# Kernel optimization log

Hardware: AMD Instinct MI355X
Metric: run time of the kernel (lower is better)

Reference implementation:

```python
import jax, jax.numpy as jnp
import numpy as np

CHUNK = 4096
DECAY = 0.99
EPS = 1e-5


def setup_inputs() -> dict:
    key = jax.random.key(0)
    k1, k2, k3, k4 = jax.random.split(key, 4)
    z = jax.random.normal(k1, (32, 64, 32, 32), dtype=jnp.float32)
    codebook = jax.random.normal(k2, (8192, 64), dtype=jnp.float32)
    cluster_size = jax.random.uniform(k3, (8192,), dtype=jnp.float32)
    embed_avg = jax.random.normal(k4, (8192, 64), dtype=jnp.float32)
    return {"z": z, "codebook": codebook, "cluster_size": cluster_size, "embed_avg": embed_avg}


def _nearest_indices(vectors, codebook):
    """Chunked fp32 squared-L2 nearest-neighbor search (matches _nearest_indices)."""
    cb = codebook.astype(jnp.float32)
    c2 = jnp.sum(cb * cb, axis=1)  # [K]

    def chunk_fn(chunk):
        v = chunk.astype(jnp.float32)  # [CHUNK, D]
        d = jnp.sum(v * v, axis=1, keepdims=True) + c2[None, :] - 2.0 * (v @ cb.T)
        return jnp.argmin(d, axis=1)

    n, d = vectors.shape  # n divisible by CHUNK by construction
    chunks = vectors.reshape(n // CHUNK, CHUNK, d)
    return jax.lax.map(chunk_fn, chunks).reshape(-1)


def reference(z, codebook, cluster_size, embed_avg):
    B, C, H, W = z.shape
    K = codebook.shape[0]
    # [B,C,H,W] -> [N,C]
    vectors = jnp.transpose(z, (0, 2, 3, 1)).reshape(-1, C)
    N = vectors.shape[0]

    indices = _nearest_indices(vectors, codebook)  # [N] int
    quantized = jnp.transpose(codebook[indices].reshape(B, H, W, C), (0, 3, 1, 2))

    # commitment loss (codebook learned via EMA, so only encoder side differentiable)
    vq_loss = jnp.mean((jax.lax.stop_gradient(quantized) - z) ** 2)
    # straight-through estimator
    quantized_st = z + jax.lax.stop_gradient(quantized - z)

    # code usage statistics
    counts = jax.ops.segment_sum(jnp.ones((N,), jnp.float32), indices, num_segments=K)
    avg_probs = counts / N
    perplexity = jnp.exp(-jnp.sum(avg_probs * jnp.log(avg_probs + 1e-10)))
    active_codes = jnp.sum(counts > 0).astype(jnp.int32)

    # EMA update (scatter-add accumulation + Laplace-smoothed normalization)
    sums = jax.ops.segment_sum(vectors.astype(jnp.float32), indices, num_segments=K)
    new_cluster_size = DECAY * cluster_size + (1.0 - DECAY) * counts
    new_embed_avg = DECAY * embed_avg + (1.0 - DECAY) * sums
    n_total = jnp.sum(new_cluster_size)
    smoothed = (new_cluster_size + EPS) / (n_total + K * EPS) * n_total
    new_codebook = new_embed_avg / smoothed[:, None]

    return (quantized_st, indices, vq_loss, perplexity, active_codes,
            new_codebook, new_cluster_size, new_embed_avg)
```

## Files before the change

### kernel.cpp

```cpp
#include <hip/hip_runtime.h>
#include <math.h>

typedef unsigned short u16;
typedef unsigned int u32;
typedef unsigned long long u64;
typedef __attribute__((ext_vector_type(8))) short short8;
typedef __attribute__((ext_vector_type(4))) float f32x4;

#define NVEC   32768
#define DIMV   64
#define KC     8192
#define NKCH   8
#define CHK    1024
#define HW     1024
#define BPLANE 65536
#define NSTEP  (CHK / 32)

#define OFF_Q    0
#define OFF_IDX  2097152
#define OFF_LOSS 2129920
#define OFF_PPL  2129921
#define OFF_ACT  2129922
#define OFF_NCB  2129923
#define OFF_NCS  2654211
#define OFF_NEA  2662403

#define WS_COUNTS 0
#define WS_SCAL   8192
#define WS_C2     8200
#define WS_MINP   16400
#define WS_OFFS   81936
#define WS_PERM   90128
#define WS_CBF    122896

__device__ __forceinline__ u16 f2bf(float x) {
    u32 u = __float_as_uint(x);
    u += 0x7fffu + ((u >> 16) & 1u);
    return (u16)(u >> 16);
}
__device__ __forceinline__ float bf2f(u16 h) {
    return __uint_as_float(((u32)h) << 16);
}
__device__ __forceinline__ u32 fmono(float f) {
    u32 b = __float_as_uint(f);
    return (b & 0x80000000u) ? ~b : (b | 0x80000000u);
}

__global__ __launch_bounds__(256) void cbsplit_kernel(const float* __restrict__ cb,
                                                      u16* __restrict__ cbf,
                                                      float* __restrict__ c2,
                                                      float* __restrict__ counts,
                                                      float* __restrict__ scal,
                                                      u64* __restrict__ minp) {
    const int t = threadIdx.x;
    const int gid = blockIdx.x * 256 + t;
    if (gid < 8192) counts[gid] = 0.f;
    if (gid < 8) scal[gid] = 0.f;
    if (gid < NVEC) minp[gid] = ~0ull;

    const int k = blockIdx.x * 4 + (t >> 6);
    const int d = t & 63;
    const int idx = k * DIMV + d;
    float x = cb[idx];
    u16 hb = f2bf(x);  float fh = bf2f(hb);
    float r1 = x - fh; u16 mb = f2bf(r1); float fm = bf2f(mb);
    float r2 = r1 - fm; u16 lb = f2bf(r2);
    const int ti = k >> 4, row = k & 15;
    const int half = d >> 5;
    const int cg = (d >> 3) & 3;
    const int le = row + cg * 16;
    u16* base = cbf + (size_t)ti * 3072 + le * 8 + (d & 7);
    base[(0 + half) * 512] = hb;
    base[(2 + half) * 512] = mb;
    base[(4 + half) * 512] = lb;
    float s = x * x;
    for (int off = 32; off > 0; off >>= 1) s += __shfl_down(s, off, 64);
    if (d == 0) c2[k] = s;
}

#define NN_COMPUTE(Bh0, Bh1, Bm0, Bm1, Bl0, Bl1, CM, NTI)                          \
    _Pragma("unroll")                                                               \
    for (int i = 0; i < 2; ++i) {                                                   \
        f32x4 acc = {CM, CM, CM, CM};                                               \
        acc = __builtin_amdgcn_mfma_f32_16x16x32_bf16(A[i][0][0], Bh0, acc, 0, 0, 0);\
        acc = __builtin_amdgcn_mfma_f32_16x16x32_bf16(A[i][0][1], Bh1, acc, 0, 0, 0);\
        acc = __builtin_amdgcn_mfma_f32_16x16x32_bf16(A[i][1][0], Bh0, acc, 0, 0, 0);\
        acc = __builtin_amdgcn_mfma_f32_16x16x32_bf16(A[i][1][1], Bh1, acc, 0, 0, 0);\
        acc = __builtin_amdgcn_mfma_f32_16x16x32_bf16(A[i][0][0], Bm0, acc, 0, 0, 0);\
        acc = __builtin_amdgcn_mfma_f32_16x16x32_bf16(A[i][0][1], Bm1, acc, 0, 0, 0);\
        acc = __builtin_amdgcn_mfma_f32_16x16x32_bf16(A[i][1][0], Bm0, acc, 0, 0, 0);\
        acc = __builtin_amdgcn_mfma_f32_16x16x32_bf16(A[i][1][1], Bm1, acc, 0, 0, 0);\
        acc = __builtin_amdgcn_mfma_f32_16x16x32_bf16(A[i][2][0], Bh0, acc, 0, 0, 0);\
        acc = __builtin_amdgcn_mfma_f32_16x16x32_bf16(A[i][2][1], Bh1, acc, 0, 0, 0);\
        acc = __builtin_amdgcn_mfma_f32_16x16x32_bf16(A[i][0][0], Bl0, acc, 0, 0, 0);\
        acc = __builtin_amdgcn_mfma_f32_16x16x32_bf16(A[i][0][1], Bl1, acc, 0, 0, 0);\
        _Pragma("unroll")                                                           \
        for (int r = 0; r < 4; ++r) {                                               \
            float a = acc[r];                                                       \
            if (a > bestv[i][r]) { bestv[i][r] = a; bestn[i][r] = (NTI); }          \
        }                                                                           \
    }

#define STAGE(B, ST)                                                                \
    _Pragma("unroll")                                                               \
    for (int j = 0; j < 3; ++j) {                                                   \
        const u16* gs = pcbf + (size_t)(ST) * 6144 + j * 2048 + tl * 8;             \
        u16* ld = &ldsb[B][j * 2048 + wv * 512];                                    \
        __builtin_amdgcn_global_load_lds(                                           \
            (const __attribute__((address_space(1))) void*)gs,                      \
            (__attribute__((address_space(3))) void*)ld, 16, 0, 0);                 \
    }

__global__ __launch_bounds__(256, 4) void nn_kernel(const float* __restrict__ z,
                                                    const u16* __restrict__ cbf,
                                                    const float* __restrict__ c2,
                                                    u64* __restrict__ minp) {
    __shared__ __align__(16) u16 ldsb[2][6144];
    const int tl = threadIdx.x;
    const int l  = tl & 63;
    const int wv = tl >> 6;
    const int vg = blockIdx.x;
    const int kc = blockIdx.y;
    const int m0 = vg * 128 + wv * 32;
    const int lr = l & 15;
    const int lg = l >> 4;

    short8 A[2][3][2];
#pragma unroll
    for (int i = 0; i < 2; ++i) {
        const int vec = m0 + i * 16 + lr;
        const float* zp = z + (size_t)(vec >> 10) * BPLANE + (vec & 1023);
#pragma unroll
        for (int s = 0; s < 2; ++s) {
            short8 ah, am, al;
#pragma unroll
            for (int e = 0; e < 8; ++e) {
                const int k = s * 32 + lg * 8 + e;
                float x = zp[k * HW];
                u16 hb = f2bf(x);   float fh = bf2f(hb);
                float r1 = x - fh;  u16 mb = f2bf(r1); float fm = bf2f(mb);
                float r2 = r1 - fm; u16 lb = f2bf(r2);
                ah[e] = (short)hb; am[e] = (short)mb; al[e] = (short)lb;
            }
            A[i][0][s] = ah; A[i][1][s] = am; A[i][2][s] = al;
        }
    }

    float bestv[2][4];
    int   bestn[2][4];
#pragma unroll
    for (int i = 0; i < 2; ++i)
#pragma unroll
        for (int r = 0; r < 4; ++r) { bestv[i][r] = -3.4e38f; bestn[i][r] = 0; }

    const int code_base = kc * CHK;
    const float* pc2 = c2 + code_base + lr;
    const u16* pcbf = cbf + (size_t)kc * (CHK / 16) * 3072;

    STAGE(0, 0)
    __syncthreads();

    for (int st = 0; st < NSTEP; ++st) {
        const int b = st & 1;
        const float cmA = -0.5f * pc2[(st * 2) * 16];
        const float cmB = -0.5f * pc2[(st * 2 + 1) * 16];
        if (st + 1 < NSTEP) { STAGE(b ^ 1, st + 1) }

        const u16* baseA = &ldsb[b][l * 8];
        {
            short8 h0 = *(const short8*)(baseA);
            short8 h1 = *(const short8*)(baseA + 512);
            short8 m0f = *(const short8*)(baseA + 1024);
            short8 m1f = *(const short8*)(baseA + 1536);
            short8 l0f = *(const short8*)(baseA + 2048);
            short8 l1f = *(const short8*)(baseA + 2560);
            NN_COMPUTE(h0, h1, m0f, m1f, l0f, l1f, cmA, st * 2)
        }
        {
            const u16* baseB = baseA + 3072;
            short8 h0 = *(const short8*)(baseB);
            short8 h1 = *(const short8*)(baseB + 512);
            short8 m0f = *(const short8*)(baseB + 1024);
            short8 m1f = *(const short8*)(baseB + 1536);
            short8 l0f = *(const short8*)(baseB + 2048);
            short8 l1f = *(const short8*)(baseB + 2560);
            NN_COMPUTE(h0, h1, m0f, m1f, l0f, l1f, cmB, st * 2 + 1)
        }
        __syncthreads();
    }

#pragma unroll
    for (int i = 0; i < 2; ++i)
#pragma unroll
        for (int r = 0; r < 4; ++r) {
            float v = bestv[i][r];
            int idx = bestn[i][r] * 16 + lr;
#pragma unroll
            for (int mk = 1; mk < 16; mk <<= 1) {
                float ov = __shfl_xor(v, mk, 64);
                int   oi = __shfl_xor(idx, mk, 64);
                if (ov > v || (ov == v && oi < idx)) { v = ov; idx = oi; }
            }
            if (lr == 0) {
                const int vec = m0 + i * 16 + lg * 4 + r;
                const u64 pack = ((u64)fmono(-v) << 32) | (u32)(code_base + idx);
                atomicMin(&minp[vec], pack);
            }
        }
}

__global__ __launch_bounds__(256) void gather_kernel(const float* __restrict__ z,
                                                     const float* __restrict__ cb,
                                                     const u64* __restrict__ minp,
                                                     float* __restrict__ out,
                                                     float* __restrict__ counts,
                                                     float* __restrict__ scal) {
    const int n = blockIdx.x * 256 + threadIdx.x;
    const int bi = (int)(u32)(minp[n] & 0xFFFFFFFFu);
    out[OFF_IDX + n] = (float)bi;
    atomicAdd(&counts[bi], 1.0f);

    const int b = n >> 10, h = n & 1023;
    const float* zp = z + (size_t)b * BPLANE + h;
    const float* cp = cb + (size_t)bi * DIMV;
    float* qp = out + OFF_Q + (size_t)b * BPLANE + h;
    float acc = 0.f;
#pragma unroll
    for (int c = 0; c < DIMV; ++c) {
        float zv = zp[c * HW];
        float q = cp[c];
        float df = q - zv;
        acc = fmaf(df, df, acc);
        qp[c * HW] = zv + df;
    }
    for (int off = 32; off > 0; off >>= 1) acc += __shfl_down(acc, off, 64);
    __shared__ float red[4];
    if ((threadIdx.x & 63) == 0) red[threadIdx.x >> 6] = acc;
    __syncthreads();
    if (threadIdx.x == 0) atomicAdd(&scal[0], (red[0] + red[1]) + (red[2] + red[3]));
}

__global__ __launch_bounds__(256) void prefix_kernel(const float* __restrict__ counts,
                                                     const float* __restrict__ cs,
                                                     float* __restrict__ out,
                                                     int* __restrict__ offs,
                                                     float* __restrict__ scal) {
    __shared__ int part[256];
    __shared__ float r0[4], r1[4], r2[4];
    const int t = threadIdx.x;
    const int base = t * 32;
    int loc[32];
    int s = 0;
    float sncs = 0.f, spl = 0.f, sact = 0.f;
#pragma unroll
    for (int j = 0; j < 32; ++j) {
        const int c = (int)counts[base + j];
        loc[j] = s; s += c;
        const float cnt = (float)c;
        const float ncs = 0.99f * cs[base + j] + 0.01f * cnt;
        out[OFF_NCS + base + j] = ncs;
        const float p = cnt * (1.0f / 32768.0f);
        spl += p * logf(p + 1e-10f);
        sact += (cnt > 0) ? 1.f : 0.f;
        sncs += ncs;
    }
    part[t] = s;
    __syncthreads();
    for (int off = 1; off < 256; off <<= 1) {
        int v = (t >= off) ? part[t - off] : 0;
        __syncthreads();
        part[t] += v;
        __syncthreads();
    }
    const int excl = part[t] - s;
#pragma unroll
    for (int j = 0; j < 32; ++j) offs[base + j] = excl + loc[j];

    for (int off = 32; off > 0; off >>= 1) {
        sncs += __shfl_down(sncs, off, 64);
        spl  += __shfl_down(spl,  off, 64);
        sact += __shfl_down(sact, off, 64);
    }
    const int w = t >> 6;
    if ((t & 63) == 0) { r0[w] = sncs; r1[w] = spl; r2[w] = sact; }
    __syncthreads();
    if (t == 0) {
        scal[1] = (r0[0] + r0[1]) + (r0[2] + r0[3]);
        scal[2] = (r1[0] + r1[1]) + (r1[2] + r1[3]);
        scal[3] = (r2[0] + r2[1]) + (r2[2] + r2[3]);
    }
}

__global__ __launch_bounds__(256) void scatter_kernel(const float* __restrict__ outIdx,
                                                      int* __restrict__ offs,
                                                      int* __restrict__ perm) {
    const int n = blockIdx.x * 256 + threadIdx.x;
    const int bi = (int)outIdx[n];
    const int pos = atomicAdd(&offs[bi], 1);
    perm[pos] = n;
}

__global__ __launch_bounds__(256) void segsum_kernel(const float* __restrict__ z,
                                                     const float* __restrict__ counts,
                                                     const int* __restrict__ offs,
                                                     const int* __restrict__ perm,
                                                     float* __restrict__ sums) {
    const int w = threadIdx.x >> 6;
    const int c = threadIdx.x & 63;
    const int k = blockIdx.x * 4 + w;
    const int end = offs[k];
    const int cnt = (int)counts[k];
    float s = 0.f;
    for (int m = end - cnt; m < end; ++m) {
        const int n = perm[m];
        s += z[(size_t)(n >> 10) * BPLANE + (size_t)c * HW + (n & 1023)];
    }
    sums[k * DIMV + c] = s;
}

__global__ __launch_bounds__(256) void final_kernel(const float* __restrict__ ea,
                                                    const float* __restrict__ sums,
                                                    float* __restrict__ out,
                                                    const float* __restrict__ scal) {
    const int i = blockIdx.x * 256 + threadIdx.x;
    const float nea = 0.99f * ea[i] + 0.01f * sums[i];
    out[OFF_NEA + i] = nea;
    const float nt = scal[1];
    const int k = i >> 6;
    const float ncs = out[OFF_NCS + k];
    const float sm = ((ncs + 1e-5f) / (nt + 0.08192f)) * nt;
    out[OFF_NCB + i] = nea / sm;
    if (i == 0) {
        out[OFF_LOSS] = scal[0] * (1.0f / 2097152.0f);
        out[OFF_PPL]  = expf(-scal[2]);
        out[OFF_ACT]  = scal[3];
    }
}

extern "C" void kernel_launch(void* const* d_in, const int* in_sizes, int n_in,
                              void* d_out, int out_size, void* d_ws, size_t ws_size,
                              hipStream_t stream) {
    const float* z  = (const float*)d_in[0];
    const float* cb = (const float*)d_in[1];
    const float* cs = (const float*)d_in[2];
    const float* ea = (const float*)d_in[3];
    float* out = (float*)d_out;
    float* ws  = (float*)d_ws;

    float* counts = ws + WS_COUNTS;
    float* scal   = ws + WS_SCAL;
    float* c2     = ws + WS_C2;
    u64*   minp   = (u64*)(ws + WS_MINP);
    int*   offs   = (int*)(ws + WS_OFFS);
    int*   perm   = (int*)(ws + WS_PERM);
    u16*   cbf    = (u16*)(ws + WS_CBF);
    float* sums   = ws + WS_CBF;

    cbsplit_kernel<<<KC / 4, 256, 0, stream>>>(cb, cbf, c2, counts, scal, minp);
    nn_kernel<<<dim3(256, NKCH), 256, 0, stream>>>(z, cbf, c2, minp);
    gather_kernel<<<NVEC / 256, 256, 0, stream>>>(z, cb, minp, out, counts, scal);
    prefix_kernel<<<1, 256, 0, stream>>>(counts, cs, out, offs, scal);
    scatter_kernel<<<NVEC / 256, 256, 0, stream>>>(out + OFF_IDX, offs, perm);
    segsum_kernel<<<KC / 4, 256, 0, stream>>>(z, counts, offs, perm, sums);
    final_kernel<<<524288 / 256, 256, 0, stream>>>(ea, sums, out, scal);
}
```

Baseline: 251.5 us.

## Double NN codebook stage depth and fuse final EMA epilogue into segsum

The nearest-neighbour kernel now stages 64 codes per LDS buffer instead of 32. This halves the number of loop iterations and barriers, but doubles LDS use and lowers the launch-bounds occupancy hint from 4 to 3. The final normalization kernel is folded into segsum_kernel, so the separate sums buffer and one launch go away. The scalar outputs (loss, perplexity, active codes) are now written by the prefix kernel. The risks are lower occupancy and higher register pressure in the hot NN loop.

```diff
diff --git a/kernel.cpp b/kernel.cpp
--- a/kernel.cpp
+++ b/kernel.cpp
@@ -14,7 +14,7 @@
 #define CHK    1024
 #define HW     1024
 #define BPLANE 65536
-#define NSTEP  (CHK / 32)
+#define NSTEP  (CHK / 64)
 
 #define OFF_Q    0
 #define OFF_IDX  2097152
@@ -103,19 +103,32 @@
 
 #define STAGE(B, ST)                                                                \
     _Pragma("unroll")                                                               \
-    for (int j = 0; j < 3; ++j) {                                                   \
-        const u16* gs = pcbf + (size_t)(ST) * 6144 + j * 2048 + tl * 8;             \
+    for (int j = 0; j < 6; ++j) {                                                   \
+        const u16* gs = pcbf + (size_t)(ST) * 12288 + j * 2048 + tl * 8;            \
         u16* ld = &ldsb[B][j * 2048 + wv * 512];                                    \
         __builtin_amdgcn_global_load_lds(                                           \
             (const __attribute__((address_space(1))) void*)gs,                      \
             (__attribute__((address_space(3))) void*)ld, 16, 0, 0);                 \
     }
 
-__global__ __launch_bounds__(256, 4) void nn_kernel(const float* __restrict__ z,
+#define SUBTILE(OFF, Q)                                                             \
+    {                                                                               \
+        const u16* bb = base0 + (OFF);                                              \
+        short8 h0  = *(const short8*)(bb);                                          \
+        short8 h1  = *(const short8*)(bb + 512);                                    \
+        short8 m0f = *(const short8*)(bb + 1024);                                   \
+        short8 m1f = *(const short8*)(bb + 1536);                                   \
+        short8 l0f = *(const short8*)(bb + 2048);                                   \
+        short8 l1f = *(const short8*)(bb + 2560);                                   \
+        const float cm = -0.5f * pc2[(st * 4 + (Q)) * 16];                          \
+        NN_COMPUTE(h0, h1, m0f, m1f, l0f, l1f, cm, st * 4 + (Q))                    \
+    }
+
+__global__ __launch_bounds__(256, 3) void nn_kernel(const float* __restrict__ z,
                                                     const u16* __restrict__ cbf,
                                                     const float* __restrict__ c2,
                                                     u64* __restrict__ minp) {
-    __shared__ __align__(16) u16 ldsb[2][6144];
+    __shared__ __align__(16) u16 ldsb[2][12288];
     const int tl = threadIdx.x;
     const int l  = tl & 63;
     const int wv = tl >> 6;
@@ -162,30 +175,12 @@
 
     for (int st = 0; st < NSTEP; ++st) {
         const int b = st & 1;
-        const float cmA = -0.5f * pc2[(st * 2) * 16];
-        const float cmB = -0.5f * pc2[(st * 2 + 1) * 16];
         if (st + 1 < NSTEP) { STAGE(b ^ 1, st + 1) }
-
-        const u16* baseA = &ldsb[b][l * 8];
-        {
-            short8 h0 = *(const short8*)(baseA);
-            short8 h1 = *(const short8*)(baseA + 512);
-            short8 m0f = *(const short8*)(baseA + 1024);
-            short8 m1f = *(const short8*)(baseA + 1536);
-            short8 l0f = *(const short8*)(baseA + 2048);
-            short8 l1f = *(const short8*)(baseA + 2560);
-            NN_COMPUTE(h0, h1, m0f, m1f, l0f, l1f, cmA, st * 2)
-        }
-        {
-            const u16* baseB = baseA + 3072;
-            short8 h0 = *(const short8*)(baseB);
-            short8 h1 = *(const short8*)(baseB + 512);
-            short8 m0f = *(const short8*)(baseB + 1024);
-            short8 m1f = *(const short8*)(baseB + 1536);
-            short8 l0f = *(const short8*)(baseB + 2048);
-            short8 l1f = *(const short8*)(baseB + 2560);
-            NN_COMPUTE(h0, h1, m0f, m1f, l0f, l1f, cmB, st * 2 + 1)
-        }
+        const u16* base0 = &ldsb[b][l * 8];
+        SUBTILE(0, 0)
+        SUBTILE(3072, 1)
+        SUBTILE(6144, 2)
+        SUBTILE(9216, 3)
         __syncthreads();
     }
 
@@ -285,9 +280,11 @@
     if ((t & 63) == 0) { r0[w] = sncs; r1[w] = spl; r2[w] = sact; }
     __syncthreads();
     if (t == 0) {
-        scal[1] = (r0[0] + r0[1]) + (r0[2] + r0[3]);
-        scal[2] = (r1[0] + r1[1]) + (r1[2] + r1[3]);
-        scal[3] = (r2[0] + r2[1]) + (r2[2] + r2[3]);
+        const float nt = (r0[0] + r0[1]) + (r0[2] + r0[3]);
+        scal[1] = nt;
+        out[OFF_LOSS] = scal[0] * (1.0f / 2097152.0f);
+        out[OFF_PPL]  = expf(-((r1[0] + r1[1]) + (r1[2] + r1[3])));
+        out[OFF_ACT]  = (r2[0] + r2[1]) + (r2[2] + r2[3]);
     }
 }
 
@@ -304,7 +301,9 @@
                                                      const float* __restrict__ counts,
                                                      const int* __restrict__ offs,
                                                      const int* __restrict__ perm,
-                                                     float* __restrict__ sums) {
+                                                     const float* __restrict__ ea,
+                                                     float* __restrict__ out,
+                                                     const float* __restrict__ scal) {
     const int w = threadIdx.x >> 6;
     const int c = threadIdx.x & 63;
     const int k = blockIdx.x * 4 + w;
@@ -315,26 +314,13 @@
         const int n = perm[m];
         s += z[(size_t)(n >> 10) * BPLANE + (size_t)c * HW + (n & 1023)];
     }
-    sums[k * DIMV + c] = s;
-}
-
-__global__ __launch_bounds__(256) void final_kernel(const float* __restrict__ ea,
-                                                    const float* __restrict__ sums,
-                                                    float* __restrict__ out,
-                                                    const float* __restrict__ scal) {
-    const int i = blockIdx.x * 256 + threadIdx.x;
-    const float nea = 0.99f * ea[i] + 0.01f * sums[i];
-    out[OFF_NEA + i] = nea;
+    const int idx = k * DIMV + c;
+    const float nea = 0.99f * ea[idx] + 0.01f * s;
+    out[OFF_NEA + idx] = nea;
     const float nt = scal[1];
-    const int k = i >> 6;
     const float ncs = out[OFF_NCS + k];
     const float sm = ((ncs + 1e-5f) / (nt + 0.08192f)) * nt;
-    out[OFF_NCB + i] = nea / sm;
-    if (i == 0) {
-        out[OFF_LOSS] = scal[0] * (1.0f / 2097152.0f);
-        out[OFF_PPL]  = expf(-scal[2]);
-        out[OFF_ACT]  = scal[3];
-    }
+    out[OFF_NCB + idx] = nea / sm;
 }
 
 extern "C" void kernel_launch(void* const* d_in, const int* in_sizes, int n_in,
@@ -354,13 +340,11 @@
     int*   offs   = (int*)(ws + WS_OFFS);
     int*   perm   = (int*)(ws + WS_PERM);
     u16*   cbf    = (u16*)(ws + WS_CBF);
-    float* sums   = ws + WS_CBF;
 
     cbsplit_kernel<<<KC / 4, 256, 0, stream>>>(cb, cbf, c2, counts, scal, minp);
     nn_kernel<<<dim3(256, NKCH), 256, 0, stream>>>(z, cbf, c2, minp);
     gather_kernel<<<NVEC / 256, 256, 0, stream>>>(z, cb, minp, out, counts, scal);
     prefix_kernel<<<1, 256, 0, stream>>>(counts, cs, out, offs, scal);
     scatter_kernel<<<NVEC / 256, 256, 0, stream>>>(out + OFF_IDX, offs, perm);
-    segsum_kernel<<<KC / 4, 256, 0, stream>>>(z, counts, offs, perm, sums);
-    final_kernel<<<524288 / 256, 256, 0, stream>>>(ea, sums, out, scal);
-}
+    segsum_kernel<<<KC / 4, 256, 0, stream>>>(z, counts, offs, perm, ea, out, scal);
+}
```

Result: no change. 255.9 us (+1.7%).
